# Kernel tuning notes

Hardware: AMD Instinct MI355X
Metric: run time of the kernel (lower is better)

Reference implementation:

```python
import jax, jax.numpy as jnp
import numpy as np

WIN = 7  # window_size
NUM_HEADS = 8


def _relative_position_index(ws: int) -> np.ndarray:
    # Matches torch.meshgrid default ('ij') indexing used in the module.
    coords = np.stack(np.meshgrid(np.arange(ws), np.arange(ws), indexing='ij'))  # (2, ws, ws)
    flat = coords.reshape(2, -1)                                   # (2, ws*ws)
    rel = flat[:, :, None] - flat[:, None, :]                      # (2, N, N)
    rel = rel.transpose(1, 2, 0).copy()                            # (N, N, 2)
    rel[:, :, 0] += ws - 1
    rel[:, :, 1] += ws - 1
    rel[:, :, 0] *= 2 * ws - 1
    return rel.sum(-1)                                             # (N, N) int


def setup_inputs() -> dict:
    key = jax.random.key(0)
    ks = jax.random.split(key, 7)
    B_, N, C = 4096, WIN * WIN, 256
    nW = 64
    return {
        'x': jax.random.normal(ks[0], (B_, N, C), dtype=jnp.float32),
        'mask': jax.random.normal(ks[1], (nW, N, N), dtype=jnp.float32),
        'qkv_w': jax.random.normal(ks[2], (3 * C, C), dtype=jnp.float32) * 0.02,
        'qkv_b': jax.random.normal(ks[3], (3 * C,), dtype=jnp.float32) * 0.02,
        'proj_w': jax.random.normal(ks[4], (C, C), dtype=jnp.float32) * 0.02,
        'proj_b': jax.random.normal(ks[5], (C,), dtype=jnp.float32) * 0.02,
        'rpb_table': jax.random.normal(ks[6], ((2 * WIN - 1) ** 2, NUM_HEADS), dtype=jnp.float32) * 0.02,
    }


def reference(x, mask, qkv_w, qkv_b, proj_w, proj_b, rpb_table):
    B_, N, C = x.shape
    H = NUM_HEADS
    hd = C // H
    scale = hd ** -0.5
    rpi = jnp.asarray(_relative_position_index(WIN))  # (N, N) int, constant

    qkv = x @ qkv_w.T + qkv_b                          # (B_, N, 3C)
    qkv = qkv.reshape(B_, N, 3, H, hd).transpose(2, 0, 3, 1, 4)  # (3, B_, H, N, hd)
    q, k, v = qkv[0], qkv[1], qkv[2]

    attn = jnp.einsum('bhnd,bhmd->bhnm', q * scale, k)  # (B_, H, N, N)
    bias = rpb_table[rpi.reshape(-1)].reshape(N, N, H).transpose(2, 0, 1)  # (H, N, N)
    attn = attn + bias[None]

    nW = mask.shape[0]
    attn = attn.reshape(B_ // nW, nW, H, N, N) + mask[None, :, None]
    attn = attn.reshape(B_, H, N, N)
    attn = jax.nn.softmax(attn, axis=-1)

    out = jnp.einsum('bhnm,bhmd->bhnd', attn, v)       # (B_, H, N, hd)
    out = out.transpose(0, 2, 1, 3).reshape(B_, N, C)
    return out @ proj_w.T + proj_b
```

## Files before the change

kernel.cpp:

```cpp
#include <hip/hip_runtime.h>

#define SEG 51380224

typedef __attribute__((ext_vector_type(8))) __bf16 bf16x8;
typedef __attribute__((ext_vector_type(4))) __bf16 bf16x4;
typedef __attribute__((ext_vector_type(4))) float f32x4;

static __device__ __forceinline__ bf16x8 bzero8() {
    bf16x8 z;
#pragma unroll
    for (int u = 0; u < 8; ++u) z[u] = (__bf16)0.0f;
    return z;
}

__global__ __launch_bounds__(256)
void cvt_bf16_k(const float* __restrict__ src, __bf16* __restrict__ dst, int n8)
{
    int i = blockIdx.x * 256 + threadIdx.x;
    const int stride = gridDim.x * 256;
    for (; i < n8; i += stride) {
        float4 a = *reinterpret_cast<const float4*>(src + (size_t)i * 8);
        float4 b = *reinterpret_cast<const float4*>(src + (size_t)i * 8 + 4);
        bf16x8 o;
        o[0] = (__bf16)a.x; o[1] = (__bf16)a.y; o[2] = (__bf16)a.z; o[3] = (__bf16)a.w;
        o[4] = (__bf16)b.x; o[5] = (__bf16)b.y; o[6] = (__bf16)b.z; o[7] = (__bf16)b.w;
        *reinterpret_cast<bf16x8*>(dst + (size_t)i * 8) = o;
    }
}

__global__ __launch_bounds__(256)
void expand_add_k(const float* __restrict__ mask, const float* __restrict__ rpb,
                  float* __restrict__ add)
{
    const int wh = blockIdx.x;
    const int w = wh >> 3, h = wh & 7;
    for (int e = threadIdx.x; e < 4096; e += 256) {
        int i = e >> 6, j = e & 63;
        float v = -1e30f;
        if (i < 49 && j < 49) {
            int ih = i / 7, iw = i - ih * 7;
            int jh = j / 7, jw = j - jh * 7;
            int bidx = (ih - jh + 6) * 13 + (iw - jw + 6);
            v = mask[(size_t)w * 2401 + i * 49 + j] + rpb[bidx * 8 + h];
        }
        add[(size_t)wh * 4096 + e] = v;
    }
}

__global__ __launch_bounds__(256)
void qkv_gemm_k(const __bf16* __restrict__ x, const __bf16* __restrict__ w,
                const float* __restrict__ bvec, __bf16* __restrict__ ws)
{
    __shared__ __bf16 As[64][72];
    __shared__ __bf16 Bs[64][72];
    const int tid  = threadIdx.x;
    const int m0   = blockIdx.x * 64;
    const int n0   = blockIdx.y * 64;
    const int wave = tid >> 6, lane = tid & 63;
    const int wm   = wave >> 1, wn = wave & 1;
    const int quad = lane >> 4, lm = lane & 15;

    f32x4 acc[2][2] = {};

    for (int k0 = 0; k0 < 256; k0 += 64) {
#pragma unroll
        for (int t = 0; t < 2; ++t) {
            int g = tid + t * 256;
            int r = g >> 3, c8 = (g & 7) << 3;
            *reinterpret_cast<bf16x8*>(&As[r][c8]) =
                *reinterpret_cast<const bf16x8*>(x + (size_t)(m0 + r) * 256 + k0 + c8);
            *reinterpret_cast<bf16x8*>(&Bs[r][c8]) =
                *reinterpret_cast<const bf16x8*>(w + (size_t)(n0 + r) * 256 + k0 + c8);
        }
        __syncthreads();
#pragma unroll
        for (int kk = 0; kk < 64; kk += 32) {
            bf16x8 a0 = *reinterpret_cast<const bf16x8*>(&As[wm*32      + lm][kk + quad*8]);
            bf16x8 a1 = *reinterpret_cast<const bf16x8*>(&As[wm*32 + 16 + lm][kk + quad*8]);
            bf16x8 b0 = *reinterpret_cast<const bf16x8*>(&Bs[wn*32      + lm][kk + quad*8]);
            bf16x8 b1 = *reinterpret_cast<const bf16x8*>(&Bs[wn*32 + 16 + lm][kk + quad*8]);
            acc[0][0] = __builtin_amdgcn_mfma_f32_16x16x32_bf16(a0, b0, acc[0][0], 0, 0, 0);
            acc[0][1] = __builtin_amdgcn_mfma_f32_16x16x32_bf16(a0, b1, acc[0][1], 0, 0, 0);
            acc[1][0] = __builtin_amdgcn_mfma_f32_16x16x32_bf16(a1, b0, acc[1][0], 0, 0, 0);
            acc[1][1] = __builtin_amdgcn_mfma_f32_16x16x32_bf16(a1, b1, acc[1][1], 0, 0, 0);
        }
        __syncthreads();
    }

#pragma unroll
    for (int mt = 0; mt < 2; ++mt)
#pragma unroll
        for (int nt = 0; nt < 2; ++nt) {
            int j  = n0 + wn*32 + nt*16 + lm;
            int c3 = j >> 8, hh = (j >> 5) & 7, d = j & 31;
            float bj  = bvec[j];
            float scl = (c3 == 0) ? 0.17677669529663687f : 1.0f;
#pragma unroll
            for (int r = 0; r < 4; ++r) {
                int m = m0 + wm*32 + mt*16 + quad*4 + r;
                int b = m / 49, nw = m - b * 49;
                float v = (acc[mt][nt][r] + bj) * scl;
                ws[(size_t)c3 * SEG + ((size_t)((b*8 + hh)*49 + nw))*32 + d] = (__bf16)v;
            }
        }
}

__global__ __launch_bounds__(64)
void attn_mfma_k(const __bf16* __restrict__ ws, const float* __restrict__ add,
                 __bf16* __restrict__ pre)
{
    __shared__ __bf16 Pl[64 * 72];
    __shared__ __bf16 Vt[32 * 72];
    const int lane = threadIdx.x;
    const int bh   = blockIdx.x;
    const int b    = bh >> 3, h = bh & 7;
    const int wh   = ((b & 63) << 3) | h;
    const int quad = lane >> 4, lm = lane & 15;
    const int koff = quad * 8;

    const __bf16* qp = ws + (size_t)bh * (49 * 32);
    const __bf16* kp = qp + SEG;
    const __bf16* vp = qp + (size_t)2 * SEG;

    {
        int d = lane >> 1, j0 = 48 + (lane & 1) * 8;
        *reinterpret_cast<bf16x8*>(&Vt[d * 72 + j0]) = bzero8();
    }
#pragma unroll
    for (int t = 0; t < 4; ++t) {
        int idx = lane + t * 64;
        if (idx < 196) {
            int j = idx >> 2, c8 = (idx & 3) * 8;
            bf16x8 vv = *reinterpret_cast<const bf16x8*>(vp + j * 32 + c8);
#pragma unroll
            for (int u = 0; u < 8; ++u) Vt[(c8 + u) * 72 + j] = vv[u];
        }
    }

    bf16x8 qf[4], kf[4];
#pragma unroll
    for (int t = 0; t < 4; ++t)
        qf[t] = *reinterpret_cast<const bf16x8*>(qp + (t * 16 + lm) * 32 + koff);
#pragma unroll
    for (int t = 0; t < 4; ++t) {
        int m = t * 16 + lm;
        kf[t] = (m < 49) ? *reinterpret_cast<const bf16x8*>(kp + m * 32 + koff)
                         : bzero8();
    }

    f32x4 s[4][4] = {};
#pragma unroll
    for (int mt = 0; mt < 4; ++mt)
#pragma unroll
        for (int nt = 0; nt < 4; ++nt)
            s[mt][nt] = __builtin_amdgcn_mfma_f32_16x16x32_bf16(kf[mt], qf[nt], s[mt][nt], 0, 0, 0);

    const float* ap = add + (size_t)wh * 4096;
#pragma unroll
    for (int nt = 0; nt < 4; ++nt) {
        int i = nt * 16 + lm;
#pragma unroll
        for (int mt = 0; mt < 4; ++mt) {
            f32x4 a4 = *reinterpret_cast<const f32x4*>(ap + i * 64 + mt * 16 + quad * 4);
            s[mt][nt] += a4;
        }
    }

#pragma unroll
    for (int nt = 0; nt < 4; ++nt) {
        float mx = -3.0e38f;
#pragma unroll
        for (int mt = 0; mt < 4; ++mt)
#pragma unroll
            for (int r = 0; r < 4; ++r) mx = fmaxf(mx, s[mt][nt][r]);
        mx = fmaxf(mx, __shfl_xor(mx, 16));
        mx = fmaxf(mx, __shfl_xor(mx, 32));
        float sum = 0.f;
#pragma unroll
        for (int mt = 0; mt < 4; ++mt)
#pragma unroll
            for (int r = 0; r < 4; ++r) {
                float e = __expf(s[mt][nt][r] - mx);
                s[mt][nt][r] = e; sum += e;
            }
        sum += __shfl_xor(sum, 16);
        sum += __shfl_xor(sum, 32);
        float rl = 1.0f / sum;
#pragma unroll
        for (int mt = 0; mt < 4; ++mt)
#pragma unroll
            for (int r = 0; r < 4; ++r) s[mt][nt][r] *= rl;
    }

#pragma unroll
    for (int nt = 0; nt < 4; ++nt) {
        int i = nt * 16 + lm;
#pragma unroll
        for (int mt = 0; mt < 4; ++mt) {
            bf16x4 p4;
#pragma unroll
            for (int r = 0; r < 4; ++r) p4[r] = (__bf16)s[mt][nt][r];
            *reinterpret_cast<bf16x4*>(&Pl[i * 72 + mt * 16 + quad * 4]) = p4;
        }
    }
    __syncthreads();

    f32x4 o[4][2] = {};
#pragma unroll
    for (int kt = 0; kt < 2; ++kt) {
        bf16x8 vf[2];
#pragma unroll
        for (int dt = 0; dt < 2; ++dt)
            vf[dt] = *reinterpret_cast<const bf16x8*>(&Vt[(dt * 16 + lm) * 72 + kt * 32 + koff]);
#pragma unroll
        for (int mt2 = 0; mt2 < 4; ++mt2) {
            bf16x8 pf = *reinterpret_cast<const bf16x8*>(&Pl[(mt2 * 16 + lm) * 72 + kt * 32 + koff]);
#pragma unroll
            for (int dt = 0; dt < 2; ++dt)
                o[mt2][dt] = __builtin_amdgcn_mfma_f32_16x16x32_bf16(pf, vf[dt], o[mt2][dt], 0, 0, 0);
        }
    }

#pragma unroll
    for (int mt2 = 0; mt2 < 4; ++mt2) {
        int ib = mt2 * 16 + quad * 4;
#pragma unroll
        for (int r = 0; r < 4; ++r) {
            int i = ib + r;
            if (i < 49) {
                size_t base = ((size_t)(b * 49 + i)) * 256 + h * 32;
                pre[base + lm]      = (__bf16)o[mt2][0][r];
                pre[base + 16 + lm] = (__bf16)o[mt2][1][r];
            }
        }
    }
}

__global__ __launch_bounds__(256)
void proj_gemm_k(const __bf16* __restrict__ pre, const __bf16* __restrict__ w,
                 const float* __restrict__ bvec, float* __restrict__ out)
{
    __shared__ __bf16 As[64][72];
    __shared__ __bf16 Bs[64][72];
    const int tid  = threadIdx.x;
    const int m0   = blockIdx.x * 64;
    const int n0   = blockIdx.y * 64;
    const int wave = tid >> 6, lane = tid & 63;
    const int wm   = wave >> 1, wn = wave & 1;
    const int quad = lane >> 4, lm = lane & 15;

    f32x4 acc[2][2] = {};

    for (int k0 = 0; k0 < 256; k0 += 64) {
#pragma unroll
        for (int t = 0; t < 2; ++t) {
            int g = tid + t * 256;
            int r = g >> 3, c8 = (g & 7) << 3;
            *reinterpret_cast<bf16x8*>(&As[r][c8]) =
                *reinterpret_cast<const bf16x8*>(pre + (size_t)(m0 + r) * 256 + k0 + c8);
            *reinterpret_cast<bf16x8*>(&Bs[r][c8]) =
                *reinterpret_cast<const bf16x8*>(w + (size_t)(n0 + r) * 256 + k0 + c8);
        }
        __syncthreads();
#pragma unroll
        for (int kk = 0; kk < 64; kk += 32) {
            bf16x8 a0 = *reinterpret_cast<const bf16x8*>(&As[wm*32      + lm][kk + quad*8]);
            bf16x8 a1 = *reinterpret_cast<const bf16x8*>(&As[wm*32 + 16 + lm][kk + quad*8]);
            bf16x8 b0 = *reinterpret_cast<const bf16x8*>(&Bs[wn*32      + lm][kk + quad*8]);
            bf16x8 b1 = *reinterpret_cast<const bf16x8*>(&Bs[wn*32 + 16 + lm][kk + quad*8]);
            acc[0][0] = __builtin_amdgcn_mfma_f32_16x16x32_bf16(a0, b0, acc[0][0], 0, 0, 0);
            acc[0][1] = __builtin_amdgcn_mfma_f32_16x16x32_bf16(a0, b1, acc[0][1], 0, 0, 0);
            acc[1][0] = __builtin_amdgcn_mfma_f32_16x16x32_bf16(a1, b0, acc[1][0], 0, 0, 0);
            acc[1][1] = __builtin_amdgcn_mfma_f32_16x16x32_bf16(a1, b1, acc[1][1], 0, 0, 0);
        }
        __syncthreads();
    }

#pragma unroll
    for (int mt = 0; mt < 2; ++mt)
#pragma unroll
        for (int nt = 0; nt < 2; ++nt) {
            int j = n0 + wn*32 + nt*16 + lm;
            float bj = bvec[j];
#pragma unroll
            for (int r = 0; r < 4; ++r) {
                int m = m0 + wm*32 + mt*16 + quad*4 + r;
                out[(size_t)m*256 + j] = acc[mt][nt][r] + bj;
            }
        }
}

extern "C" void kernel_launch(void* const* d_in, const int* in_sizes, int n_in,
                              void* d_out, int out_size, void* d_ws, size_t ws_size,
                              hipStream_t stream)
{
    const float* x      = (const float*)d_in[0];
    const float* mask   = (const float*)d_in[1];
    const float* qkv_w  = (const float*)d_in[2];
    const float* qkv_b  = (const float*)d_in[3];
    const float* proj_w = (const float*)d_in[4];
    const float* proj_b = (const float*)d_in[5];
    const float* rpb    = (const float*)d_in[6];

    __bf16* ws  = (__bf16*)d_ws;
    __bf16* pre = ws + (size_t)3 * SEG;
    float*  out = (float*)d_out;

    char*   ob      = (char*)d_out;
    float*  addbuf  = (float*)ob;
    __bf16* qkv_wb  = (__bf16*)(ob + (10u << 20));
    __bf16* xb      = (__bf16*)(ob + (16u << 20));
    __bf16* proj_wb = ws;

    cvt_bf16_k<<<dim3(2048), 256, 0, stream>>>(x, xb, 51380224 / 8);
    cvt_bf16_k<<<dim3(96),   256, 0, stream>>>(qkv_w, qkv_wb, 196608 / 8);
    expand_add_k<<<dim3(512), 256, 0, stream>>>(mask, rpb, addbuf);
    qkv_gemm_k<<<dim3(3136, 12), 256, 0, stream>>>(xb, qkv_wb, qkv_b, ws);
    attn_mfma_k<<<dim3(32768), 64, 0, stream>>>(ws, addbuf, pre);
    cvt_bf16_k<<<dim3(32),   256, 0, stream>>>(proj_w, proj_wb, 65536 / 8);
    proj_gemm_k<<<dim3(3136, 4), 256, 0, stream>>>(pre, proj_wb, proj_b, out);
}
```

Baseline: 793.1 us.

## Enlarge GEMM tiles to 128x128 with direct global-to-LDS loads and XCD swizzle

Both the QKV and projection GEMMs move from 64x64 to 128x128 output tiles, with each wave computing a 64x64 sub-tile from a 4x4 grid of MFMA accumulators. Operand tiles are copied straight from global memory into LDS with the global_load_lds builtin, so the data no longer passes through registers. Block indices are remapped across the eight XCDs so that neighbouring tiles share L2. The goal is more data reuse per LDS load and less load overhead, at the cost of more accumulator registers and an unpadded LDS layout that may cause bank conflicts.

```diff
diff --git a/kernel.cpp b/kernel.cpp
--- a/kernel.cpp
+++ b/kernel.cpp
@@ -11,6 +11,12 @@
 #pragma unroll
     for (int u = 0; u < 8; ++u) z[u] = (__bf16)0.0f;
     return z;
+}
+
+static __device__ __forceinline__ void gl_lds16(const __bf16* g, __bf16* l) {
+    __builtin_amdgcn_global_load_lds(
+        (const __attribute__((address_space(1))) void*)g,
+        (__attribute__((address_space(3))) void*)l, 16, 0, 0);
 }
 
 __global__ __launch_bounds__(256)
@@ -51,58 +57,69 @@
 void qkv_gemm_k(const __bf16* __restrict__ x, const __bf16* __restrict__ w,
                 const float* __restrict__ bvec, __bf16* __restrict__ ws)
 {
-    __shared__ __bf16 As[64][72];
-    __shared__ __bf16 Bs[64][72];
+    __shared__ __bf16 As[128][64];
+    __shared__ __bf16 Bs[128][64];
     const int tid  = threadIdx.x;
-    const int m0   = blockIdx.x * 64;
-    const int n0   = blockIdx.y * 64;
+    const int nwg  = 1568 * 6;
+    const int bid  = blockIdx.x;
+    const int v    = (bid & 7) * (nwg >> 3) + (bid >> 3);
+    const int mb   = v / 6, nb = v - mb * 6;
+    const int m0   = mb * 128;
+    const int n0   = nb * 128;
     const int wave = tid >> 6, lane = tid & 63;
     const int wm   = wave >> 1, wn = wave & 1;
     const int quad = lane >> 4, lm = lane & 15;
-
-    f32x4 acc[2][2] = {};
+    const int koff = quad * 8;
+
+    const int srow = wave * 8 + (lane >> 3);
+    const int scol = (lane & 7) * 8;
+
+    f32x4 acc[4][4] = {};
 
     for (int k0 = 0; k0 < 256; k0 += 64) {
 #pragma unroll
-        for (int t = 0; t < 2; ++t) {
-            int g = tid + t * 256;
-            int r = g >> 3, c8 = (g & 7) << 3;
-            *reinterpret_cast<bf16x8*>(&As[r][c8]) =
-                *reinterpret_cast<const bf16x8*>(x + (size_t)(m0 + r) * 256 + k0 + c8);
-            *reinterpret_cast<bf16x8*>(&Bs[r][c8]) =
-                *reinterpret_cast<const bf16x8*>(w + (size_t)(n0 + r) * 256 + k0 + c8);
+        for (int i = 0; i < 4; ++i) {
+            int row = i * 32 + srow;
+            gl_lds16(x + (size_t)(m0 + row) * 256 + k0 + scol,
+                     &As[0][0] + i * 2048 + wave * 512);
+            gl_lds16(w + (size_t)(n0 + row) * 256 + k0 + scol,
+                     &Bs[0][0] + i * 2048 + wave * 512);
         }
         __syncthreads();
 #pragma unroll
         for (int kk = 0; kk < 64; kk += 32) {
-            bf16x8 a0 = *reinterpret_cast<const bf16x8*>(&As[wm*32      + lm][kk + quad*8]);
-            bf16x8 a1 = *reinterpret_cast<const bf16x8*>(&As[wm*32 + 16 + lm][kk + quad*8]);
-            bf16x8 b0 = *reinterpret_cast<const bf16x8*>(&Bs[wn*32      + lm][kk + quad*8]);
-            bf16x8 b1 = *reinterpret_cast<const bf16x8*>(&Bs[wn*32 + 16 + lm][kk + quad*8]);
-            acc[0][0] = __builtin_amdgcn_mfma_f32_16x16x32_bf16(a0, b0, acc[0][0], 0, 0, 0);
-            acc[0][1] = __builtin_amdgcn_mfma_f32_16x16x32_bf16(a0, b1, acc[0][1], 0, 0, 0);
-            acc[1][0] = __builtin_amdgcn_mfma_f32_16x16x32_bf16(a1, b0, acc[1][0], 0, 0, 0);
-            acc[1][1] = __builtin_amdgcn_mfma_f32_16x16x32_bf16(a1, b1, acc[1][1], 0, 0, 0);
+            bf16x8 af[4], bfr[4];
+#pragma unroll
+            for (int mt = 0; mt < 4; ++mt)
+                af[mt] = *reinterpret_cast<const bf16x8*>(&As[wm*64 + mt*16 + lm][kk + koff]);
+#pragma unroll
+            for (int nt = 0; nt < 4; ++nt)
+                bfr[nt] = *reinterpret_cast<const bf16x8*>(&Bs[wn*64 + nt*16 + lm][kk + koff]);
+#pragma unroll
+            for (int mt = 0; mt < 4; ++mt)
+#pragma unroll
+                for (int nt = 0; nt < 4; ++nt)
+                    acc[mt][nt] = __builtin_amdgcn_mfma_f32_16x16x32_bf16(af[mt], bfr[nt], acc[mt][nt], 0, 0, 0);
         }
         __syncthreads();
     }
 
 #pragma unroll
-    for (int mt = 0; mt < 2; ++mt)
-#pragma unroll
-        for (int nt = 0; nt < 2; ++nt) {
-            int j  = n0 + wn*32 + nt*16 + lm;
-            int c3 = j >> 8, hh = (j >> 5) & 7, d = j & 31;
-            float bj  = bvec[j];
-            float scl = (c3 == 0) ? 0.17677669529663687f : 1.0f;
+    for (int nt = 0; nt < 4; ++nt) {
+        int j  = n0 + wn*64 + nt*16 + lm;
+        int c3 = j >> 8, hh = (j >> 5) & 7, d = j & 31;
+        float bj  = bvec[j];
+        float scl = (c3 == 0) ? 0.17677669529663687f : 1.0f;
+#pragma unroll
+        for (int mt = 0; mt < 4; ++mt)
 #pragma unroll
             for (int r = 0; r < 4; ++r) {
-                int m = m0 + wm*32 + mt*16 + quad*4 + r;
+                int m = m0 + wm*64 + mt*16 + quad*4 + r;
                 int b = m / 49, nw = m - b * 49;
-                float v = (acc[mt][nt][r] + bj) * scl;
-                ws[(size_t)c3 * SEG + ((size_t)((b*8 + hh)*49 + nw))*32 + d] = (__bf16)v;
+                float vv = (acc[mt][nt][r] + bj) * scl;
+                ws[(size_t)c3 * SEG + ((size_t)((b*8 + hh)*49 + nw))*32 + d] = (__bf16)vv;
             }
-        }
+    }
 }
 
 __global__ __launch_bounds__(64)
@@ -240,54 +257,65 @@
 void proj_gemm_k(const __bf16* __restrict__ pre, const __bf16* __restrict__ w,
                  const float* __restrict__ bvec, float* __restrict__ out)
 {
-    __shared__ __bf16 As[64][72];
-    __shared__ __bf16 Bs[64][72];
+    __shared__ __bf16 As[128][64];
+    __shared__ __bf16 Bs[128][64];
     const int tid  = threadIdx.x;
-    const int m0   = blockIdx.x * 64;
-    const int n0   = blockIdx.y * 64;
+    const int nwg  = 1568 * 2;
+    const int bid  = blockIdx.x;
+    const int v    = (bid & 7) * (nwg >> 3) + (bid >> 3);
+    const int mb   = v >> 1, nb = v & 1;
+    const int m0   = mb * 128;
+    const int n0   = nb * 128;
     const int wave = tid >> 6, lane = tid & 63;
     const int wm   = wave >> 1, wn = wave & 1;
     const int quad = lane >> 4, lm = lane & 15;
-
-    f32x4 acc[2][2] = {};
+    const int koff = quad * 8;
+
+    const int srow = wave * 8 + (lane >> 3);
+    const int scol = (lane & 7) * 8;
+
+    f32x4 acc[4][4] = {};
 
     for (int k0 = 0; k0 < 256; k0 += 64) {
 #pragma unroll
-        for (int t = 0; t < 2; ++t) {
-            int g = tid + t * 256;
-            int r = g >> 3, c8 = (g & 7) << 3;
-            *reinterpret_cast<bf16x8*>(&As[r][c8]) =
-                *reinterpret_cast<const bf16x8*>(pre + (size_t)(m0 + r) * 256 + k0 + c8);
-            *reinterpret_cast<bf16x8*>(&Bs[r][c8]) =
-                *reinterpret_cast<const bf16x8*>(w + (size_t)(n0 + r) * 256 + k0 + c8);
+        for (int i = 0; i < 4; ++i) {
+            int row = i * 32 + srow;
+            gl_lds16(pre + (size_t)(m0 + row) * 256 + k0 + scol,
+                     &As[0][0] + i * 2048 + wave * 512);
+            gl_lds16(w + (size_t)(n0 + row) * 256 + k0 + scol,
+                     &Bs[0][0] + i * 2048 + wave * 512);
         }
         __syncthreads();
 #pragma unroll
         for (int kk = 0; kk < 64; kk += 32) {
-            bf16x8 a0 = *reinterpret_cast<const bf16x8*>(&As[wm*32      + lm][kk + quad*8]);
-            bf16x8 a1 = *reinterpret_cast<const bf16x8*>(&As[wm*32 + 16 + lm][kk + quad*8]);
-            bf16x8 b0 = *reinterpret_cast<const bf16x8*>(&Bs[wn*32      + lm][kk + quad*8]);
-            bf16x8 b1 = *reinterpret_cast<const bf16x8*>(&Bs[wn*32 + 16 + lm][kk + quad*8]);
-            acc[0][0] = __builtin_amdgcn_mfma_f32_16x16x32_bf16(a0, b0, acc[0][0], 0, 0, 0);
-            acc[0][1] = __builtin_amdgcn_mfma_f32_16x16x32_bf16(a0, b1, acc[0][1], 0, 0, 0);
-            acc[1][0] = __builtin_amdgcn_mfma_f32_16x16x32_bf16(a1, b0, acc[1][0], 0, 0, 0);
-            acc[1][1] = __builtin_amdgcn_mfma_f32_16x16x32_bf16(a1, b1, acc[1][1], 0, 0, 0);
+            bf16x8 af[4], bfr[4];
+#pragma unroll
+            for (int mt = 0; mt < 4; ++mt)
+                af[mt] = *reinterpret_cast<const bf16x8*>(&As[wm*64 + mt*16 + lm][kk + koff]);
+#pragma unroll
+            for (int nt = 0; nt < 4; ++nt)
+                bfr[nt] = *reinterpret_cast<const bf16x8*>(&Bs[wn*64 + nt*16 + lm][kk + koff]);
+#pragma unroll
+            for (int mt = 0; mt < 4; ++mt)
+#pragma unroll
+                for (int nt = 0; nt < 4; ++nt)
+                    acc[mt][nt] = __builtin_amdgcn_mfma_f32_16x16x32_bf16(af[mt], bfr[nt], acc[mt][nt], 0, 0, 0);
         }
         __syncthreads();
     }
 
 #pragma unroll
-    for (int mt = 0; mt < 2; ++mt)
-#pragma unroll
-        for (int nt = 0; nt < 2; ++nt) {
-            int j = n0 + wn*32 + nt*16 + lm;
-            float bj = bvec[j];
+    for (int nt = 0; nt < 4; ++nt) {
+        int j = n0 + wn*64 + nt*16 + lm;
+        float bj = bvec[j];
+#pragma unroll
+        for (int mt = 0; mt < 4; ++mt)
 #pragma unroll
             for (int r = 0; r < 4; ++r) {
-                int m = m0 + wm*32 + mt*16 + quad*4 + r;
+                int m = m0 + wm*64 + mt*16 + quad*4 + r;
                 out[(size_t)m*256 + j] = acc[mt][nt][r] + bj;
             }
-        }
+    }
 }
 
 extern "C" void kernel_launch(void* const* d_in, const int* in_sizes, int n_in,
@@ -315,8 +343,8 @@
     cvt_bf16_k<<<dim3(2048), 256, 0, stream>>>(x, xb, 51380224 / 8);
     cvt_bf16_k<<<dim3(96),   256, 0, stream>>>(qkv_w, qkv_wb, 196608 / 8);
     expand_add_k<<<dim3(512), 256, 0, stream>>>(mask, rpb, addbuf);
-    qkv_gemm_k<<<dim3(3136, 12), 256, 0, stream>>>(xb, qkv_wb, qkv_b, ws);
+    qkv_gemm_k<<<dim3(1568 * 6), 256, 0, stream>>>(xb, qkv_wb, qkv_b, ws);
     attn_mfma_k<<<dim3(32768), 64, 0, stream>>>(ws, addbuf, pre);
     cvt_bf16_k<<<dim3(32),   256, 0, stream>>>(proj_w, proj_wb, 65536 / 8);
-    proj_gemm_k<<<dim3(3136, 4), 256, 0, stream>>>(pre, proj_wb, proj_b, out);
-}
+    proj_gemm_k<<<dim3(1568 * 2), 256, 0, stream>>>(pre, proj_wb, proj_b, out);
+}
```

Result: no change. 782.6 us (-1.3%).
